# Optimization experiments

Measured on AMD Instinct MI355X. Metric: run time of the kernel, lower is better.

Reference implementation:

```python
import math
import jax, jax.numpy as jnp
import numpy as np

B, S, D, H, FF, L = 2, 1024, 1024, 16, 4096, 4
HD = D // H
EPS = 1e-5


def setup_inputs() -> dict:
    key = jax.random.key(0)
    ks = jax.random.split(key, 14)
    sd = 0.02
    inp = {
        "x": jax.random.normal(ks[0], (B, S, D), jnp.float32),
        "mask": jnp.zeros((S, S), jnp.float32),
        "Wqkv": jax.random.normal(ks[1], (L, D, 3 * D), jnp.float32) * sd,
        "bqkv": jnp.zeros((L, 3 * D), jnp.float32),
        "Wo": jax.random.normal(ks[2], (L, D, D), jnp.float32) * sd,
        "bo": jnp.zeros((L, D), jnp.float32),
        "g1": jnp.ones((L, D), jnp.float32),
        "be1": jnp.zeros((L, D), jnp.float32),
        "W1": jax.random.normal(ks[3], (L, D, FF), jnp.float32) * sd,
        "bf1": jnp.zeros((L, FF), jnp.float32),
        "W2": jax.random.normal(ks[4], (L, FF, D), jnp.float32) * sd,
        "bf2": jnp.zeros((L, D), jnp.float32),
        "g2": jnp.ones((L, D), jnp.float32),
        "be2": jnp.zeros((L, D), jnp.float32),
    }
    return inp


def _layer_norm(x, g, b):
    # biased variance, matching the torch LayerNormalization module
    mean = jnp.mean(x, axis=-1, keepdims=True)
    var = jnp.mean((x - mean) ** 2, axis=-1, keepdims=True)
    return g * (x - mean) / jnp.sqrt(var + EPS) + b


def _encoder(x, mask, params):
    inv_sqrt_dk = 1.0 / math.sqrt(HD)

    def step(h, p):
        Wqkv, bqkv, Wo, bo, g1, be1, W1, bf1, W2, bf2, g2, be2 = p
        b, s, d = h.shape
        qkv = h @ Wqkv + bqkv                         # [B,S,3D]
        qkv = qkv.reshape(b, s, H, 3 * HD).transpose(0, 2, 1, 3)  # [B,H,S,3hd]
        q, k, v = jnp.split(qkv, 3, axis=-1)          # each [B,H,S,hd]
        scores = jnp.einsum("bhqd,bhkd->bhqk", q, k) * inv_sqrt_dk + mask
        attn = jax.nn.softmax(scores, axis=-1)
        vals = jnp.einsum("bhqk,bhkd->bhqd", attn, v)
        vals = vals.transpose(0, 2, 1, 3).reshape(b, s, d)
        a = vals @ Wo + bo
        h = _layer_norm(h + a, g1, be1)
        f = jax.nn.relu(h @ W1 + bf1) @ W2 + bf2
        h = _layer_norm(h + f, g2, be2)
        return h, None

    out, _ = jax.lax.scan(step, x, params)
    return out


def reference(x, mask, Wqkv, bqkv, Wo, bo, g1, be1, W1, bf1, W2, bf2, g2, be2):
    params = (Wqkv, bqkv, Wo, bo, g1, be1, W1, bf1, W2, bf2, g2, be2)
    return _encoder(x, mask, params)
```

## Files before the change

### kernel.cpp

```cpp
#include <hip/hip_runtime.h>
#include <hip/hip_bf16.h>
#include <cmath>

typedef __attribute__((ext_vector_type(8))) short short8;
typedef __attribute__((ext_vector_type(4))) short short4v;
typedef __attribute__((ext_vector_type(4))) float f32x4;

#define EPI_QKV 0
#define EPI_RELU 2
#define EPI_PART 3

__device__ __forceinline__ void gl2lds16(const void* g, void* l) {
  __builtin_amdgcn_global_load_lds(
      (const __attribute__((address_space(1))) unsigned int*)g,
      (__attribute__((address_space(3))) unsigned int*)l, 16, 0, 0);
}

template <int EPI>
__global__ __launch_bounds__(256) void gemm_k(
    const __hip_bfloat16* __restrict__ A, const __hip_bfloat16* __restrict__ WT,
    const float* __restrict__ bias, float* __restrict__ outF,
    __hip_bfloat16* __restrict__ outB, __hip_bfloat16* __restrict__ Qo,
    __hip_bfloat16* __restrict__ Ko, __hip_bfloat16* __restrict__ VTo, int M,
    int N, int K, int P) {
  __shared__ __align__(16) __hip_bfloat16 Alds[128 * 32];
  __shared__ __align__(16) __hip_bfloat16 Blds[128 * 32];
  const int tid = threadIdx.x;
  const int nbn = N >> 7;
  const int npb = (M >> 7) * nbn;
  const int nwg = gridDim.x;
  const int cpx = nwg >> 3;
  const int bid = blockIdx.x;
  const int wg = (bid & 7) * cpx + (bid >> 3);
  const int part = wg / npb;
  const int wgl = wg - part * npb;
  const int bm = wgl / nbn, bn = wgl - bm * nbn;
  const int brow = bm << 7, bcol = bn << 7;
  const int lane = tid & 63;
  const int wid = tid >> 6;
  const int wm = wid >> 1, wn = wid & 1;
  const int lr = lane & 15, lk = lane >> 4;
  const int Kp = K / P;
  const int k0 = part * Kp;

  f32x4 acc[4][4] = {};

  const int srow = tid >> 2;
  const int ssw = (tid >> 3) & 3;
  const int scol = (((tid & 3) ^ ssw) << 3);
  const __hip_bfloat16* aptr = A + (size_t)(brow + srow) * K + scol + k0;
  const __hip_bfloat16* bptr = WT + (size_t)(bcol + srow) * K + scol + k0;
  __hip_bfloat16* la = &Alds[tid * 8];
  __hip_bfloat16* lb = &Blds[tid * 8];
  const size_t K64 = (size_t)64 * K;
  const int fsw = (lr >> 1) & 3;

  for (int kt = 0; kt < Kp; kt += 32) {
    gl2lds16(aptr + kt, la);
    gl2lds16(aptr + K64 + kt, la + 2048);
    gl2lds16(bptr + kt, lb);
    gl2lds16(bptr + K64 + kt, lb + 2048);
    __syncthreads();
    short8 af[4], bf[4];
#pragma unroll
    for (int m = 0; m < 4; ++m)
      af[m] = *(const short8*)&Alds[(wm * 64 + m * 16 + lr) * 32 + ((lk ^ fsw) << 3)];
#pragma unroll
    for (int n = 0; n < 4; ++n)
      bf[n] = *(const short8*)&Blds[(wn * 64 + n * 16 + lr) * 32 + ((lk ^ fsw) << 3)];
#pragma unroll
    for (int m = 0; m < 4; ++m)
#pragma unroll
      for (int n = 0; n < 4; ++n)
        acc[m][n] =
            __builtin_amdgcn_mfma_f32_16x16x32_bf16(af[m], bf[n], acc[m][n], 0, 0, 0);
    __syncthreads();
  }

#pragma unroll
  for (int n = 0; n < 4; ++n) {
    const int c = bcol + wn * 64 + n * 16 + lr;
    float bb = 0.f;
    if constexpr (EPI != EPI_PART) bb = bias[c];
#pragma unroll
    for (int m = 0; m < 4; ++m) {
#pragma unroll
      for (int r = 0; r < 4; ++r) {
        const int row = brow + wm * 64 + m * 16 + lk * 4 + r;
        float v = acc[m][n][r] + bb;
        if constexpr (EPI == EPI_PART) {
          outF[((size_t)part * M + row) * N + c] = v;
        } else if constexpr (EPI == EPI_RELU) {
          outB[(size_t)row * N + c] = __float2bfloat16(fmaxf(v, 0.f));
        } else {
          const int b = row >> 10, s = row & 1023;
          const int hh = c / 192, t = c - hh * 192;
          const size_t base = ((size_t)(b * 16 + hh) * 1024 + s) * 64;
          if (t < 64)
            Qo[base + t] = __float2bfloat16(v);
          else if (t < 128)
            Ko[base + t - 64] = __float2bfloat16(v);
          else
            VTo[((size_t)(b * 16 + hh) * 64 + (t - 128)) * 1024 + s] =
                __float2bfloat16(v);
        }
      }
    }
  }
}

__global__ __launch_bounds__(256) void attn_k(const __hip_bfloat16* __restrict__ Q,
                                              const __hip_bfloat16* __restrict__ Kx,
                                              const __hip_bfloat16* __restrict__ VT,
                                              __hip_bfloat16* __restrict__ O) {
  __shared__ __align__(16) __hip_bfloat16 P2[4][16][72];
  const int tid = threadIdx.x, lane = tid & 63, w = tid >> 6;
  const int lr = lane & 15, lk = lane >> 4;
  const int bh = blockIdx.y;
  const int q0 = blockIdx.x * 64 + w * 16;
  const __hip_bfloat16* Qb = Q + (size_t)bh * 65536;
  const __hip_bfloat16* Kb = Kx + (size_t)bh * 65536;
  const __hip_bfloat16* Vb = VT + (size_t)bh * 65536;

  short8 bq[2];
#pragma unroll
  for (int ks = 0; ks < 2; ++ks)
    bq[ks] = *(const short8*)(Qb + (size_t)(q0 + lr) * 64 + ks * 32 + lk * 8);

  float m = -INFINITY, l = 0.f;
  f32x4 oacc[4] = {};

  for (int kt = 0; kt < 1024; kt += 64) {
    f32x4 sc[4] = {};
#pragma unroll
    for (int nt = 0; nt < 4; ++nt) {
      const __hip_bfloat16* kp = Kb + (size_t)(kt + nt * 16 + lr) * 64 + lk * 8;
      short8 k0 = *(const short8*)kp;
      short8 k1 = *(const short8*)(kp + 32);
      sc[nt] = __builtin_amdgcn_mfma_f32_16x16x32_bf16(k0, bq[0], sc[nt], 0, 0, 0);
      sc[nt] = __builtin_amdgcn_mfma_f32_16x16x32_bf16(k1, bq[1], sc[nt], 0, 0, 0);
    }
    float mx = sc[0][0];
#pragma unroll
    for (int nt = 0; nt < 4; ++nt)
#pragma unroll
      for (int r = 0; r < 4; ++r) mx = fmaxf(mx, sc[nt][r]);
    mx *= 0.125f;
    mx = fmaxf(mx, __shfl_xor(mx, 16, 64));
    mx = fmaxf(mx, __shfl_xor(mx, 32, 64));
    const float mnew = fmaxf(m, mx);
    const float corr = __expf(m - mnew);
    m = mnew;
    float rs = 0.f;
#pragma unroll
    for (int nt = 0; nt < 4; ++nt)
#pragma unroll
      for (int r = 0; r < 4; ++r) {
        const float pv = __expf(sc[nt][r] * 0.125f - mnew);
        sc[nt][r] = pv;
        rs += pv;
      }
    rs += __shfl_xor(rs, 16, 64);
    rs += __shfl_xor(rs, 32, 64);
    l = l * corr + rs;
#pragma unroll
    for (int dt = 0; dt < 4; ++dt)
#pragma unroll
      for (int r = 0; r < 4; ++r) oacc[dt][r] *= corr;
#pragma unroll
    for (int nt = 0; nt < 4; ++nt) {
      short4v pk;
#pragma unroll
      for (int r = 0; r < 4; ++r)
        pk[r] = (short)__bfloat16_as_ushort(__float2bfloat16(sc[nt][r]));
      *(short4v*)&P2[w][lr][nt * 16 + lk * 4] = pk;
    }
    short8 bp[2];
#pragma unroll
    for (int kb = 0; kb < 2; ++kb)
      bp[kb] = *(const short8*)&P2[w][lr][kb * 32 + lk * 8];
#pragma unroll
    for (int dt = 0; dt < 4; ++dt) {
      const __hip_bfloat16* vp = Vb + (size_t)(dt * 16 + lr) * 1024 + kt + lk * 8;
      short8 v0 = *(const short8*)vp;
      short8 v1 = *(const short8*)(vp + 32);
      oacc[dt] = __builtin_amdgcn_mfma_f32_16x16x32_bf16(v0, bp[0], oacc[dt], 0, 0, 0);
      oacc[dt] = __builtin_amdgcn_mfma_f32_16x16x32_bf16(v1, bp[1], oacc[dt], 0, 0, 0);
    }
  }

  const int b = bh >> 4, hh = bh & 15;
  const float inv = 1.f / l;
#pragma unroll
  for (int dt = 0; dt < 4; ++dt) {
    short4v pk;
#pragma unroll
    for (int r = 0; r < 4; ++r)
      pk[r] = (short)__bfloat16_as_ushort(__float2bfloat16(oacc[dt][r] * inv));
    *(short4v*)(O + ((size_t)(b * 1024 + q0 + lr)) * 1024 + hh * 64 + dt * 16 +
                lk * 4) = pk;
  }
}

__global__ __launch_bounds__(256) void ln_red_k(
    const float* __restrict__ part, const float* __restrict__ resid,
    const float* __restrict__ bias, const float* __restrict__ g,
    const float* __restrict__ be, float* __restrict__ hf,
    __hip_bfloat16* __restrict__ hb, int P) {
  const int row = blockIdx.x, tid = threadIdx.x;
  const size_t MN = (size_t)2048 * 1024;
  float4 v = ((const float4*)(resid + (size_t)row * 1024))[tid];
  const float4 bb = ((const float4*)bias)[tid];
  v.x += bb.x; v.y += bb.y; v.z += bb.z; v.w += bb.w;
#pragma unroll 4
  for (int p = 0; p < P; ++p) {
    const float4 pv = ((const float4*)(part + p * MN + (size_t)row * 1024))[tid];
    v.x += pv.x; v.y += pv.y; v.z += pv.z; v.w += pv.w;
  }
  float s = v.x + v.y + v.z + v.w;
  float q = v.x * v.x + v.y * v.y + v.z * v.z + v.w * v.w;
#pragma unroll
  for (int off = 1; off < 64; off <<= 1) {
    s += __shfl_xor(s, off, 64);
    q += __shfl_xor(q, off, 64);
  }
  __shared__ float ss[4], qs[4];
  const int w = tid >> 6;
  if ((tid & 63) == 0) { ss[w] = s; qs[w] = q; }
  __syncthreads();
  s = ss[0] + ss[1] + ss[2] + ss[3];
  q = qs[0] + qs[1] + qs[2] + qs[3];
  const float mean = s * (1.f / 1024.f);
  const float var = fmaxf(q * (1.f / 1024.f) - mean * mean, 0.f);
  const float rstd = rsqrtf(var + 1e-5f);
  const float4 gv = ((const float4*)g)[tid];
  const float4 bv = ((const float4*)be)[tid];
  float4 o;
  o.x = gv.x * (v.x - mean) * rstd + bv.x;
  o.y = gv.y * (v.y - mean) * rstd + bv.y;
  o.z = gv.z * (v.z - mean) * rstd + bv.z;
  o.w = gv.w * (v.w - mean) * rstd + bv.w;
  ((float4*)(hf + (size_t)row * 1024))[tid] = o;
  __hip_bfloat16* hp = hb + (size_t)row * 1024 + tid * 4;
  hp[0] = __float2bfloat16(o.x);
  hp[1] = __float2bfloat16(o.y);
  hp[2] = __float2bfloat16(o.z);
  hp[3] = __float2bfloat16(o.w);
}

__global__ __launch_bounds__(256) void tconv_k(const float* __restrict__ W,
                                               __hip_bfloat16* __restrict__ WT,
                                               int K, int N) {
  __shared__ __hip_bfloat16 t[64][65];
  const int tid = threadIdx.x;
  const float* src = W + (size_t)blockIdx.z * K * N;
  __hip_bfloat16* dst = WT + (size_t)blockIdx.z * N * K;
  const int n0 = blockIdx.x << 6, k0 = blockIdx.y << 6;
#pragma unroll
  for (int i = tid; i < 1024; i += 256) {
    const int r = i >> 4, c = (i & 15) << 2;
    const float4 v = *(const float4*)(src + (size_t)(k0 + r) * N + n0 + c);
    t[r][c + 0] = __float2bfloat16(v.x);
    t[r][c + 1] = __float2bfloat16(v.y);
    t[r][c + 2] = __float2bfloat16(v.z);
    t[r][c + 3] = __float2bfloat16(v.w);
  }
  __syncthreads();
#pragma unroll
  for (int i = tid; i < 1024; i += 256) {
    const int r = i >> 4, c = (i & 15) << 2;
    __hip_bfloat16* d = dst + (size_t)(n0 + r) * K + k0 + c;
    d[0] = t[c + 0][r];
    d[1] = t[c + 1][r];
    d[2] = t[c + 2][r];
    d[3] = t[c + 3][r];
  }
}

__global__ __launch_bounds__(256) void initx_k(const float* __restrict__ x,
                                               float* __restrict__ hf,
                                               __hip_bfloat16* __restrict__ hb) {
  const int i = blockIdx.x * 256 + threadIdx.x;
  const float4 v = ((const float4*)x)[i];
  ((float4*)hf)[i] = v;
  __hip_bfloat16* hp = hb + (size_t)i * 4;
  hp[0] = __float2bfloat16(v.x);
  hp[1] = __float2bfloat16(v.y);
  hp[2] = __float2bfloat16(v.z);
  hp[3] = __float2bfloat16(v.w);
}

extern "C" void kernel_launch(void* const* d_in, const int* in_sizes, int n_in,
                              void* d_out, int out_size, void* d_ws, size_t ws_size,
                              hipStream_t stream) {
  const float* x = (const float*)d_in[0];
  const float* Wqkv = (const float*)d_in[2];
  const float* bqkv = (const float*)d_in[3];
  const float* Wo = (const float*)d_in[4];
  const float* bo = (const float*)d_in[5];
  const float* g1 = (const float*)d_in[6];
  const float* be1 = (const float*)d_in[7];
  const float* W1 = (const float*)d_in[8];
  const float* bf1 = (const float*)d_in[9];
  const float* W2 = (const float*)d_in[10];
  const float* bf2 = (const float*)d_in[11];
  const float* g2 = (const float*)d_in[12];
  const float* be2 = (const float*)d_in[13];

  char* p = (char*)d_ws;
  auto take = [&](size_t bytes) {
    char* r = p;
    p += (bytes + 255) & ~(size_t)255;
    return r;
  };
  __hip_bfloat16* WqkvT = (__hip_bfloat16*)take(12582912ull * 2);
  __hip_bfloat16* WoT = (__hip_bfloat16*)take(4194304ull * 2);
  __hip_bfloat16* W1T = (__hip_bfloat16*)take(16777216ull * 2);
  __hip_bfloat16* W2T = (__hip_bfloat16*)take(16777216ull * 2);
  float* hf = (float*)take(2097152ull * 4);
  float* partf = (float*)take(4ull * 2097152ull * 4);
  __hip_bfloat16* hb = (__hip_bfloat16*)take(2097152ull * 2);
  __hip_bfloat16* Qb = (__hip_bfloat16*)take(2097152ull * 2);
  __hip_bfloat16* Kb = (__hip_bfloat16*)take(2097152ull * 2);
  __hip_bfloat16* Vb = (__hip_bfloat16*)take(2097152ull * 2);
  __hip_bfloat16* att = (__hip_bfloat16*)take(2097152ull * 2);
  __hip_bfloat16* f1 = (__hip_bfloat16*)take(8388608ull * 2);

  tconv_k<<<dim3(48, 16, 4), 256, 0, stream>>>(Wqkv, WqkvT, 1024, 3072);
  tconv_k<<<dim3(16, 16, 4), 256, 0, stream>>>(Wo, WoT, 1024, 1024);
  tconv_k<<<dim3(64, 16, 4), 256, 0, stream>>>(W1, W1T, 1024, 4096);
  tconv_k<<<dim3(16, 64, 4), 256, 0, stream>>>(W2, W2T, 4096, 1024);
  initx_k<<<2048, 256, 0, stream>>>(x, hf, hb);

  for (int l = 0; l < 4; ++l) {
    gemm_k<EPI_QKV><<<384, 256, 0, stream>>>(
        hb, WqkvT + (size_t)l * 3145728, bqkv + l * 3072, nullptr, nullptr, Qb, Kb,
        Vb, 2048, 3072, 1024, 1);
    attn_k<<<dim3(16, 32), 256, 0, stream>>>(Qb, Kb, Vb, att);
    gemm_k<EPI_PART><<<512, 256, 0, stream>>>(
        att, WoT + (size_t)l * 1048576, nullptr, partf, nullptr, nullptr, nullptr,
        nullptr, 2048, 1024, 1024, 4);
    ln_red_k<<<2048, 256, 0, stream>>>(partf, hf, bo + l * 1024, g1 + l * 1024,
                                       be1 + l * 1024, hf, hb, 4);
    gemm_k<EPI_RELU><<<512, 256, 0, stream>>>(
        hb, W1T + (size_t)l * 4194304, bf1 + l * 4096, nullptr, f1, nullptr, nullptr,
        nullptr, 2048, 4096, 1024, 1);
    gemm_k<EPI_PART><<<512, 256, 0, stream>>>(
        f1, W2T + (size_t)l * 4194304, nullptr, partf, nullptr, nullptr, nullptr,
        nullptr, 2048, 1024, 4096, 4);
    float* lnout = (l == 3) ? (float*)d_out : hf;
    ln_red_k<<<2048, 256, 0, stream>>>(partf, hf, bf2 + l * 1024, g2 + l * 1024,
                                       be2 + l * 1024, lnout, hb, 4);
  }
}
```

Baseline: 998.5 us.

## Split attention over KV chunks and halve GEMM tile width to raise occupancy

Attention now splits the 1024 keys into four 256-key chunks, each handled by a separate workgroup. Each chunk writes unnormalized fp32 partial outputs plus its running max and sum, and a new combine kernel merges the four with log-sum-exp weights into bf16. The GEMM tile shrinks from 128x128 to 128x64 and every grid doubles, so the device gets more workgroups. The cost is an extra kernel and extra fp32 traffic for the partials, and each GEMM workgroup reuses its A tile less.

```diff
diff --git a/kernel.cpp b/kernel.cpp
--- a/kernel.cpp
+++ b/kernel.cpp
@@ -24,9 +24,9 @@
     __hip_bfloat16* __restrict__ Ko, __hip_bfloat16* __restrict__ VTo, int M,
     int N, int K, int P) {
   __shared__ __align__(16) __hip_bfloat16 Alds[128 * 32];
-  __shared__ __align__(16) __hip_bfloat16 Blds[128 * 32];
+  __shared__ __align__(16) __hip_bfloat16 Blds[64 * 32];
   const int tid = threadIdx.x;
-  const int nbn = N >> 7;
+  const int nbn = N >> 6;
   const int npb = (M >> 7) * nbn;
   const int nwg = gridDim.x;
   const int cpx = nwg >> 3;
@@ -35,7 +35,7 @@
   const int part = wg / npb;
   const int wgl = wg - part * npb;
   const int bm = wgl / nbn, bn = wgl - bm * nbn;
-  const int brow = bm << 7, bcol = bn << 7;
+  const int brow = bm << 7, bcol = bn << 6;
   const int lane = tid & 63;
   const int wid = tid >> 6;
   const int wm = wid >> 1, wn = wid & 1;
@@ -43,7 +43,7 @@
   const int Kp = K / P;
   const int k0 = part * Kp;
 
-  f32x4 acc[4][4] = {};
+  f32x4 acc[4][2] = {};
 
   const int srow = tid >> 2;
   const int ssw = (tid >> 3) & 3;
@@ -59,27 +59,26 @@
     gl2lds16(aptr + kt, la);
     gl2lds16(aptr + K64 + kt, la + 2048);
     gl2lds16(bptr + kt, lb);
-    gl2lds16(bptr + K64 + kt, lb + 2048);
     __syncthreads();
-    short8 af[4], bf[4];
+    short8 af[4], bf[2];
 #pragma unroll
     for (int m = 0; m < 4; ++m)
       af[m] = *(const short8*)&Alds[(wm * 64 + m * 16 + lr) * 32 + ((lk ^ fsw) << 3)];
 #pragma unroll
-    for (int n = 0; n < 4; ++n)
-      bf[n] = *(const short8*)&Blds[(wn * 64 + n * 16 + lr) * 32 + ((lk ^ fsw) << 3)];
+    for (int n = 0; n < 2; ++n)
+      bf[n] = *(const short8*)&Blds[(wn * 32 + n * 16 + lr) * 32 + ((lk ^ fsw) << 3)];
 #pragma unroll
     for (int m = 0; m < 4; ++m)
 #pragma unroll
-      for (int n = 0; n < 4; ++n)
+      for (int n = 0; n < 2; ++n)
         acc[m][n] =
             __builtin_amdgcn_mfma_f32_16x16x32_bf16(af[m], bf[n], acc[m][n], 0, 0, 0);
     __syncthreads();
   }
 
 #pragma unroll
-  for (int n = 0; n < 4; ++n) {
-    const int c = bcol + wn * 64 + n * 16 + lr;
+  for (int n = 0; n < 2; ++n) {
+    const int c = bcol + wn * 32 + n * 16 + lr;
     float bb = 0.f;
     if constexpr (EPI != EPI_PART) bb = bias[c];
 #pragma unroll
@@ -109,15 +108,17 @@
   }
 }
 
-__global__ __launch_bounds__(256) void attn_k(const __hip_bfloat16* __restrict__ Q,
-                                              const __hip_bfloat16* __restrict__ Kx,
-                                              const __hip_bfloat16* __restrict__ VT,
-                                              __hip_bfloat16* __restrict__ O) {
+__global__ __launch_bounds__(256, 8) void attn_k(
+    const __hip_bfloat16* __restrict__ Q, const __hip_bfloat16* __restrict__ Kx,
+    const __hip_bfloat16* __restrict__ VT, float* __restrict__ Opart,
+    float2* __restrict__ ml) {
   __shared__ __align__(16) __hip_bfloat16 P2[4][16][72];
   const int tid = threadIdx.x, lane = tid & 63, w = tid >> 6;
   const int lr = lane & 15, lk = lane >> 4;
-  const int bh = blockIdx.y;
-  const int q0 = blockIdx.x * 64 + w * 16;
+  const int bh = blockIdx.x;
+  const int q0 = blockIdx.y * 64 + w * 16;
+  const int sp = blockIdx.z;
+  const int kv0 = sp << 8;
   const __hip_bfloat16* Qb = Q + (size_t)bh * 65536;
   const __hip_bfloat16* Kb = Kx + (size_t)bh * 65536;
   const __hip_bfloat16* Vb = VT + (size_t)bh * 65536;
@@ -130,7 +131,7 @@
   float m = -INFINITY, l = 0.f;
   f32x4 oacc[4] = {};
 
-  for (int kt = 0; kt < 1024; kt += 64) {
+  for (int kt = kv0; kt < kv0 + 256; kt += 64) {
     f32x4 sc[4] = {};
 #pragma unroll
     for (int nt = 0; nt < 4; ++nt) {
@@ -189,17 +190,58 @@
     }
   }
 
+  float* Op = Opart + (((size_t)sp * 32 + bh) * 1024 + q0 + lr) * 64;
+#pragma unroll
+  for (int dt = 0; dt < 4; ++dt) *(f32x4*)(Op + dt * 16 + lk * 4) = oacc[dt];
+  if (lk == 0) {
+    float2 v;
+    v.x = m;
+    v.y = l;
+    ml[((size_t)sp * 32 + bh) * 1024 + q0 + lr] = v;
+  }
+}
+
+__global__ __launch_bounds__(256) void attn_comb_k(const float* __restrict__ Opart,
+                                                   const float2* __restrict__ ml,
+                                                   __hip_bfloat16* __restrict__ O) {
+  const int id = blockIdx.x;
+  const int bh = id >> 6;
+  const int qb = (id & 63) << 4;
+  const int tid = threadIdx.x;
+  const int r = tid >> 4;
+  const int dq = (tid & 15) << 2;
+  const int q = qb + r;
+  float2 mls[4];
+  float mstar = -INFINITY;
+#pragma unroll
+  for (int p = 0; p < 4; ++p) {
+    mls[p] = ml[((size_t)p * 32 + bh) * 1024 + q];
+    mstar = fmaxf(mstar, mls[p].x);
+  }
+  float lstar = 0.f, wgt[4];
+#pragma unroll
+  for (int p = 0; p < 4; ++p) {
+    wgt[p] = __expf(mls[p].x - mstar);
+    lstar += mls[p].y * wgt[p];
+  }
+  float4 o = {0.f, 0.f, 0.f, 0.f};
+#pragma unroll
+  for (int p = 0; p < 4; ++p) {
+    const float4 v =
+        *(const float4*)(Opart + (((size_t)p * 32 + bh) * 1024 + q) * 64 + dq);
+    o.x += v.x * wgt[p];
+    o.y += v.y * wgt[p];
+    o.z += v.z * wgt[p];
+    o.w += v.w * wgt[p];
+  }
+  const float inv = 1.f / lstar;
   const int b = bh >> 4, hh = bh & 15;
-  const float inv = 1.f / l;
-#pragma unroll
-  for (int dt = 0; dt < 4; ++dt) {
-    short4v pk;
-#pragma unroll
-    for (int r = 0; r < 4; ++r)
-      pk[r] = (short)__bfloat16_as_ushort(__float2bfloat16(oacc[dt][r] * inv));
-    *(short4v*)(O + ((size_t)(b * 1024 + q0 + lr)) * 1024 + hh * 64 + dt * 16 +
-                lk * 4) = pk;
-  }
+  short4v pk;
+  pk[0] = (short)__bfloat16_as_ushort(__float2bfloat16(o.x * inv));
+  pk[1] = (short)__bfloat16_as_ushort(__float2bfloat16(o.y * inv));
+  pk[2] = (short)__bfloat16_as_ushort(__float2bfloat16(o.z * inv));
+  pk[3] = (short)__bfloat16_as_ushort(__float2bfloat16(o.w * inv));
+  *(short4v*)(O + ((size_t)(b * 1024 + q)) * 1024 + hh * 64 + dq) = pk;
 }
 
 __global__ __launch_bounds__(256) void ln_red_k(
@@ -319,12 +361,14 @@
   __hip_bfloat16* W2T = (__hip_bfloat16*)take(16777216ull * 2);
   float* hf = (float*)take(2097152ull * 4);
   float* partf = (float*)take(4ull * 2097152ull * 4);
+  float2* mlbuf = (float2*)take(131072ull * 8);
   __hip_bfloat16* hb = (__hip_bfloat16*)take(2097152ull * 2);
   __hip_bfloat16* Qb = (__hip_bfloat16*)take(2097152ull * 2);
   __hip_bfloat16* Kb = (__hip_bfloat16*)take(2097152ull * 2);
   __hip_bfloat16* Vb = (__hip_bfloat16*)take(2097152ull * 2);
   __hip_bfloat16* att = (__hip_bfloat16*)take(2097152ull * 2);
   __hip_bfloat16* f1 = (__hip_bfloat16*)take(8388608ull * 2);
+  float* Opart = partf;
 
   tconv_k<<<dim3(48, 16, 4), 256, 0, stream>>>(Wqkv, WqkvT, 1024, 3072);
   tconv_k<<<dim3(16, 16, 4), 256, 0, stream>>>(Wo, WoT, 1024, 1024);
@@ -333,19 +377,20 @@
   initx_k<<<2048, 256, 0, stream>>>(x, hf, hb);
 
   for (int l = 0; l < 4; ++l) {
-    gemm_k<EPI_QKV><<<384, 256, 0, stream>>>(
+    gemm_k<EPI_QKV><<<768, 256, 0, stream>>>(
         hb, WqkvT + (size_t)l * 3145728, bqkv + l * 3072, nullptr, nullptr, Qb, Kb,
         Vb, 2048, 3072, 1024, 1);
-    attn_k<<<dim3(16, 32), 256, 0, stream>>>(Qb, Kb, Vb, att);
-    gemm_k<EPI_PART><<<512, 256, 0, stream>>>(
+    attn_k<<<dim3(32, 16, 4), 256, 0, stream>>>(Qb, Kb, Vb, Opart, mlbuf);
+    attn_comb_k<<<2048, 256, 0, stream>>>(Opart, mlbuf, att);
+    gemm_k<EPI_PART><<<1024, 256, 0, stream>>>(
         att, WoT + (size_t)l * 1048576, nullptr, partf, nullptr, nullptr, nullptr,
         nullptr, 2048, 1024, 1024, 4);
     ln_red_k<<<2048, 256, 0, stream>>>(partf, hf, bo + l * 1024, g1 + l * 1024,
                                        be1 + l * 1024, hf, hb, 4);
-    gemm_k<EPI_RELU><<<512, 256, 0, stream>>>(
+    gemm_k<EPI_RELU><<<1024, 256, 0, stream>>>(
         hb, W1T + (size_t)l * 4194304, bf1 + l * 4096, nullptr, f1, nullptr, nullptr,
         nullptr, 2048, 4096, 1024, 1);
-    gemm_k<EPI_PART><<<512, 256, 0, stream>>>(
+    gemm_k<EPI_PART><<<1024, 256, 0, stream>>>(
         f1, W2T + (size_t)l * 4194304, nullptr, partf, nullptr, nullptr, nullptr,
         nullptr, 2048, 1024, 4096, 4);
     float* lnout = (l == 3) ? (float*)d_out : hf;
```

Measured after the change: 1.025 ms. 2.6% more time.
